# Optimization experiments

Hardware: AMD Instinct MI355X
Metric: run time of the kernel (lower is better)

The kernel has to match this reference:

```python
import jax, jax.numpy as jnp
import numpy as np

DIM = 1024
N_HEADS = 16
HEAD_DIM = DIM // N_HEADS


def setup_inputs() -> dict:
    key = jax.random.key(0)
    ks = jax.random.split(key, 5)
    s = 1.0 / np.sqrt(DIM)
    return {
        "x": jax.random.normal(ks[0], (2, 2048, DIM), dtype=jnp.float32),
        "w_qkv": jax.random.normal(ks[1], (DIM, 3 * DIM), dtype=jnp.float32) * s,
        "b_qkv": jnp.zeros((3 * DIM,), dtype=jnp.float32),
        "w_proj": jax.random.normal(ks[2], (DIM, DIM), dtype=jnp.float32) * s,
        "b_proj": jnp.zeros((DIM,), dtype=jnp.float32),
    }


def reference(x, w_qkv, b_qkv, w_proj, b_proj):
    B, T, C = x.shape
    qkv = x @ w_qkv + b_qkv                      # [B,T,3C]
    qkv = qkv.reshape(B, T, 3, N_HEADS, HEAD_DIM)
    q, k, v = qkv[:, :, 0], qkv[:, :, 1], qkv[:, :, 2]  # [B,T,H,D]
    scale = 1.0 / np.sqrt(HEAD_DIM)
    scores = jnp.einsum("bqhd,bkhd->bhqk", q, k) * scale  # [B,H,T,T]
    attn = jax.nn.softmax(scores, axis=-1)
    out = jnp.einsum("bhqk,bkhd->bqhd", attn, v)          # [B,T,H,D]
    out = out.reshape(B, T, C)
    return out @ w_proj + b_proj
```

## Files before the change

kernel.cpp:

```cpp
#include <hip/hip_runtime.h>

typedef unsigned short u16;
typedef unsigned int   u32;
typedef __bf16 bf16x8 __attribute__((ext_vector_type(8)));
typedef float  f32x4  __attribute__((ext_vector_type(4)));
typedef float  f32x16 __attribute__((ext_vector_type(16)));

#define TSEQ 2048
#define NHEAD 16
#define HDIM 64
#define CDIM 1024
#define N3   3072
#define MROWS 4096

__device__ __forceinline__ u16 f2bf(float f) {
    union { float f; u32 u; } v; v.f = f;
    u32 r = v.u + 0x7FFFu + ((v.u >> 16) & 1u);
    return (u16)(r >> 16);
}

__device__ __forceinline__ u32 pkbf(float a, float b) {
#if __has_builtin(__builtin_amdgcn_cvt_pk_bf16_f32)
    typedef __bf16 bf16x2 __attribute__((ext_vector_type(2)));
    bf16x2 t = __builtin_amdgcn_cvt_pk_bf16_f32(a, b);
    union { bf16x2 v; u32 u; } c; c.v = t; return c.u;
#else
    return (u32)f2bf(a) | ((u32)f2bf(b) << 16);
#endif
}

__device__ __forceinline__ void gld16(const u16* g, u16* l) {
    __builtin_amdgcn_global_load_lds(
        (const __attribute__((address_space(1))) u32*)g,
        (__attribute__((address_space(3))) u32*)l, 16, 0, 0);
}

__global__ __launch_bounds__(256) void pack_bf16_kernel(const float* __restrict__ in,
                                                        u16* __restrict__ out, int n4) {
    int i = blockIdx.x * 256 + threadIdx.x;
    if (i >= n4) return;
    float4 v = reinterpret_cast<const float4*>(in)[i];
    ushort4 o;
    o.x = f2bf(v.x); o.y = f2bf(v.y); o.z = f2bf(v.z); o.w = f2bf(v.w);
    reinterpret_cast<ushort4*>(out)[i] = o;
}

__global__ __launch_bounds__(256) void transpose_pack(const float* __restrict__ in,
                                                      u16* __restrict__ out, int K, int N) {
    __shared__ float tile[32][33];
    int n0 = blockIdx.x * 32, k0 = blockIdx.y * 32;
    int tx = threadIdx.x, ty = threadIdx.y;
#pragma unroll
    for (int i = 0; i < 4; i++)
        tile[ty + i * 8][tx] = in[(size_t)(k0 + ty + i * 8) * N + n0 + tx];
    __syncthreads();
#pragma unroll
    for (int i = 0; i < 4; i++)
        out[(size_t)(n0 + ty + i * 8) * K + k0 + tx] = f2bf(tile[tx][ty + i * 8]);
}

__global__ __launch_bounds__(256) void gemm_qkv(const u16* __restrict__ A, const u16* __restrict__ Bt,
                                                const float* __restrict__ bias, u16* __restrict__ Qb,
                                                u16* __restrict__ Ksw, u16* __restrict__ Vsw) {
    __shared__ __align__(16) u16 Al[128 * 32];
    __shared__ __align__(16) u16 Bl[128 * 32];
    const int tid  = threadIdx.x;
    const int lane = tid & 63;
    const int wave = tid >> 6;
    const int wm = (wave >> 1) * 64;
    const int wn = (wave & 1) * 64;
    const int row0 = blockIdx.x * 128;
    const int col0 = blockIdx.y * 128;
    const int lr = lane & 15;
    const int lq = lane >> 4;
    const float c2 = 0.125f * 1.44269504088896f;

    f32x4 acc[4][4];
#pragma unroll
    for (int i = 0; i < 4; i++)
#pragma unroll
        for (int j = 0; j < 4; j++) acc[i][j] = f32x4{0.f, 0.f, 0.f, 0.f};

    const int sr = tid >> 2, sc_ = (tid & 3) * 8;

    for (int k0 = 0; k0 < CDIM; k0 += 32) {
#pragma unroll
        for (int s = 0; s < 2; s++) {
            int i = tid + s * 256;
            int r = sr + s * 64;
            gld16(&A[(size_t)(row0 + r) * CDIM + k0 + sc_], &Al[i * 8]);
            gld16(&Bt[(size_t)(col0 + r) * CDIM + k0 + sc_], &Bl[i * 8]);
        }
        __syncthreads();
        bf16x8 af[4], bfr[4];
#pragma unroll
        for (int t = 0; t < 4; t++) {
            af[t]  = *reinterpret_cast<const bf16x8*>(&Al[(wm + t * 16 + lr) * 32 + lq * 8]);
            bfr[t] = *reinterpret_cast<const bf16x8*>(&Bl[(wn + t * 16 + lr) * 32 + lq * 8]);
        }
#pragma unroll
        for (int mt = 0; mt < 4; mt++)
#pragma unroll
            for (int nt = 0; nt < 4; nt++)
                acc[mt][nt] = __builtin_amdgcn_mfma_f32_16x16x32_bf16(af[mt], bfr[nt], acc[mt][nt], 0, 0, 0);
        __syncthreads();
    }
#pragma unroll
    for (int mt = 0; mt < 4; mt++) {
#pragma unroll
        for (int nt = 0; nt < 4; nt++) {
            int col = col0 + wn + nt * 16 + lr;
            float bv = bias[col];
            int region = col >> 10;
            int c = col & 1023, h = c >> 6, d = c & 63;
#pragma unroll
            for (int r = 0; r < 4; r++) {
                int m = row0 + wm + mt * 16 + lq * 4 + r;
                float v = acc[mt][nt][r] + bv;
                int b  = m >> 11, t = m & 2047;
                int kb = t >> 6,  tr = t & 63;
                size_t base = (size_t)((b * 16 + h) * 32 + kb) * 4096;
                if (region == 0) {
                    Qb[(size_t)m * 1024 + col] = f2bf(v * c2);
                } else if (region == 1) {
                    Ksw[base + tr * 64 + (((d >> 3) ^ (tr & 7)) << 3) + (d & 7)] = f2bf(v);
                } else {
                    int slot = (tr >> 4) * 16 + ((tr >> 2) & 1) * 8 + (tr & 3) + ((tr >> 3) & 1) * 4;
                    Vsw[base + d * 64 + (((slot >> 3) ^ (d & 7)) << 3) + (slot & 7)] = f2bf(v);
                }
            }
        }
    }
}

__global__ __launch_bounds__(256) void gemm_proj(const u16* __restrict__ A, const u16* __restrict__ Bt,
                                                 const float* __restrict__ bias, float* __restrict__ C) {
    __shared__ __align__(16) u16 Al[64 * 32];
    __shared__ __align__(16) u16 Bl[128 * 32];
    const int tid  = threadIdx.x;
    const int lane = tid & 63;
    const int wave = tid >> 6;
    const int wm = (wave >> 1) * 32;
    const int wn = (wave & 1) * 64;
    const int row0 = blockIdx.x * 64;
    const int col0 = blockIdx.y * 128;
    const int lr = lane & 15;
    const int lq = lane >> 4;

    f32x4 acc[2][4];
#pragma unroll
    for (int i = 0; i < 2; i++)
#pragma unroll
        for (int j = 0; j < 4; j++) acc[i][j] = f32x4{0.f, 0.f, 0.f, 0.f};

    const int sr = tid >> 2, sc_ = (tid & 3) * 8;

    for (int k0 = 0; k0 < CDIM; k0 += 32) {
        gld16(&A[(size_t)(row0 + sr) * CDIM + k0 + sc_], &Al[tid * 8]);
#pragma unroll
        for (int s = 0; s < 2; s++)
            gld16(&Bt[(size_t)(col0 + sr + s * 64) * CDIM + k0 + sc_], &Bl[(tid + s * 256) * 8]);
        __syncthreads();
        bf16x8 af[2], bfr[4];
#pragma unroll
        for (int t = 0; t < 2; t++)
            af[t] = *reinterpret_cast<const bf16x8*>(&Al[(wm + t * 16 + lr) * 32 + lq * 8]);
#pragma unroll
        for (int t = 0; t < 4; t++)
            bfr[t] = *reinterpret_cast<const bf16x8*>(&Bl[(wn + t * 16 + lr) * 32 + lq * 8]);
#pragma unroll
        for (int mt = 0; mt < 2; mt++)
#pragma unroll
            for (int nt = 0; nt < 4; nt++)
                acc[mt][nt] = __builtin_amdgcn_mfma_f32_16x16x32_bf16(af[mt], bfr[nt], acc[mt][nt], 0, 0, 0);
        __syncthreads();
    }
#pragma unroll
    for (int mt = 0; mt < 2; mt++) {
#pragma unroll
        for (int nt = 0; nt < 4; nt++) {
            int col = col0 + wn + nt * 16 + lr;
            float bv = bias[col];
#pragma unroll
            for (int r = 0; r < 4; r++) {
                int row = row0 + wm + mt * 16 + lq * 4 + r;
                C[(size_t)row * CDIM + col] = acc[mt][nt][r] + bv;
            }
        }
    }
}

__global__ __launch_bounds__(256) void attn_kernel(const u16* __restrict__ Qb,
                                                   const u16* __restrict__ Ksw,
                                                   const u16* __restrict__ Vsw,
                                                   u16* __restrict__ AO) {
    __shared__ __align__(16) u16 Kl[2][64 * 64];
    __shared__ __align__(16) u16 Vl[2][64 * 64];
    const int qb = blockIdx.x, h = blockIdx.y, b = blockIdx.z;
    const int tid = threadIdx.x, lane = tid & 63, wave = tid >> 6;
    const int l31 = lane & 31, l5 = lane >> 5;
    const int q0 = qb * 128 + wave * 32;

    bf16x8 qf[4];
    {
        const u16* qp = Qb + (size_t)(b * TSEQ + q0 + l31) * CDIM + h * 64 + l5 * 8;
#pragma unroll
        for (int kc = 0; kc < 4; kc++) qf[kc] = *reinterpret_cast<const bf16x8*>(qp + kc * 16);
    }
    f32x16 o[2];
#pragma unroll
    for (int dt = 0; dt < 2; dt++)
#pragma unroll
        for (int i = 0; i < 16; i++) o[dt][i] = 0.f;
    float l = 0.f;

    const u16* ktiles = Ksw + (size_t)((b * 16 + h) * 32) * 4096;
    const u16* vtiles = Vsw + (size_t)((b * 16 + h) * 32) * 4096;
    const int soff = tid * 8;

#pragma unroll
    for (int j = 0; j < 2; j++) {
        gld16(ktiles + j * 2048 + soff, &Kl[0][j * 2048 + soff]);
        gld16(vtiles + j * 2048 + soff, &Vl[0][j * 2048 + soff]);
    }
    __syncthreads();

    for (int kb = 0; kb < TSEQ / 64; kb++) {
        const int cur = kb & 1, nxt = cur ^ 1;
        const int nkb = (kb + 1 < TSEQ / 64) ? kb + 1 : kb;
#pragma unroll
        for (int j = 0; j < 2; j++) {
            gld16(ktiles + (size_t)nkb * 4096 + j * 2048 + soff, &Kl[nxt][j * 2048 + soff]);
            gld16(vtiles + (size_t)nkb * 4096 + j * 2048 + soff, &Vl[nxt][j * 2048 + soff]);
        }
        f32x16 st[2];
#pragma unroll
        for (int nt = 0; nt < 2; nt++)
#pragma unroll
            for (int i = 0; i < 16; i++) st[nt][i] = 0.f;
#pragma unroll
        for (int kc = 0; kc < 4; kc++) {
#pragma unroll
            for (int nt = 0; nt < 2; nt++) {
                bf16x8 kf = *reinterpret_cast<const bf16x8*>(
                    &Kl[cur][(nt * 32 + l31) * 64 + (((kc * 2 + l5) ^ (l31 & 7)) << 3)]);
                st[nt] = __builtin_amdgcn_mfma_f32_32x32x16_bf16(kf, qf[kc], st[nt], 0, 0, 0);
            }
        }
        bf16x8 pa[4];
#pragma unroll
        for (int nt = 0; nt < 2; nt++) {
            float pe[16];
#pragma unroll
            for (int r = 0; r < 16; r++) {
                pe[r] = __builtin_amdgcn_exp2f(st[nt][r]);
                l += pe[r];
            }
            union { bf16x8 v; u32 w[4]; } u0, u1;
#pragma unroll
            for (int j = 0; j < 4; j++) {
                u0.w[j] = pkbf(pe[2 * j],     pe[2 * j + 1]);
                u1.w[j] = pkbf(pe[8 + 2 * j], pe[8 + 2 * j + 1]);
            }
            pa[nt * 2]     = u0.v;
            pa[nt * 2 + 1] = u1.v;
        }
#pragma unroll
        for (int c = 0; c < 4; c++) {
#pragma unroll
            for (int dt = 0; dt < 2; dt++) {
                bf16x8 vf = *reinterpret_cast<const bf16x8*>(
                    &Vl[cur][(dt * 32 + l31) * 64 + (((c * 2 + l5) ^ (l31 & 7)) << 3)]);
                o[dt] = __builtin_amdgcn_mfma_f32_32x32x16_bf16(pa[c], vf, o[dt], 0, 0, 0);
            }
        }
        __syncthreads();
    }
    l += __shfl_xor(l, 32);
    float linv = 1.0f / l;
#pragma unroll
    for (int reg = 0; reg < 16; reg++) {
        int qrow = (reg & 3) + 8 * (reg >> 2) + 4 * l5;
        float li = __shfl(linv, qrow);
#pragma unroll
        for (int dt = 0; dt < 2; dt++) {
            AO[(size_t)(b * TSEQ + q0 + qrow) * CDIM + h * 64 + dt * 32 + l31] =
                f2bf(o[dt][reg] * li);
        }
    }
}

extern "C" void kernel_launch(void* const* d_in, const int* in_sizes, int n_in,
                              void* d_out, int out_size, void* d_ws, size_t ws_size,
                              hipStream_t stream) {
    const float* x      = (const float*)d_in[0];
    const float* w_qkv  = (const float*)d_in[1];
    const float* b_qkv  = (const float*)d_in[2];
    const float* w_proj = (const float*)d_in[3];
    const float* b_proj = (const float*)d_in[4];
    float* out = (float*)d_out;

    u16* ws     = (u16*)d_ws;
    u16* Xb     = ws;
    u16* Wqkvt  = Xb + 4194304;
    u16* Wprojt = Wqkvt + 3145728;
    u16* Qb     = Wprojt + 1048576;
    u16* Ksw    = Qb + 4194304;
    u16* Vsw    = Ksw + 4194304;
    u16* AO     = Vsw + 4194304;

    pack_bf16_kernel<<<4096, 256, 0, stream>>>(x, Xb, 4194304 / 4);
    transpose_pack<<<dim3(96, 32), dim3(32, 8), 0, stream>>>(w_qkv, Wqkvt, 1024, 3072);
    transpose_pack<<<dim3(32, 32), dim3(32, 8), 0, stream>>>(w_proj, Wprojt, 1024, 1024);
    gemm_qkv<<<dim3(32, 24), 256, 0, stream>>>(Xb, Wqkvt, b_qkv, Qb, Ksw, Vsw);
    attn_kernel<<<dim3(16, 16, 2), 256, 0, stream>>>(Qb, Ksw, Vsw, AO);
    gemm_proj<<<dim3(64, 8), 256, 0, stream>>>(AO, Wprojt, b_proj, out);
}
```

Before: 199.7 us.

## Store Q/K/V in MFMA-fragment order and load attention operands directly to registers

The QKV GEMM epilogue now writes Q, K and V in a layout that matches the per-lane MFMA fragment order. This lets the attention kernel drop its LDS double-buffering and block-wide barriers and load K/V fragments straight from global memory into registers, with K prefetched one tile ahead. Each wave now reads the full K/V stream itself instead of sharing it through LDS, which raises global/L2 traffic and register pressure. The change also merges the two weight-transpose launches into one, reorders the attention grid so heads are the fastest-varying index, and adds a v_perm fallback for bf16 packing.

```diff
diff --git a/kernel.cpp b/kernel.cpp
--- a/kernel.cpp
+++ b/kernel.cpp
@@ -25,7 +25,10 @@
     bf16x2 t = __builtin_amdgcn_cvt_pk_bf16_f32(a, b);
     union { bf16x2 v; u32 u; } c; c.v = t; return c.u;
 #else
-    return (u32)f2bf(a) | ((u32)f2bf(b) << 16);
+    union { float f; u32 u; } ua, ub; ua.f = a; ub.f = b;
+    u32 sel = 0x07060302, d;
+    asm("v_perm_b32 %0, %1, %2, %3" : "=v"(d) : "v"(ub.u), "v"(ua.u), "v"(sel));
+    return d;
 #endif
 }
 
@@ -45,10 +48,15 @@
     reinterpret_cast<ushort4*>(out)[i] = o;
 }
 
-__global__ __launch_bounds__(256) void transpose_pack(const float* __restrict__ in,
-                                                      u16* __restrict__ out, int K, int N) {
+__global__ __launch_bounds__(256) void transpose_pack2(const float* __restrict__ wqkv,
+                                                       const float* __restrict__ wproj,
+                                                       u16* __restrict__ oqkv, u16* __restrict__ oproj) {
     __shared__ float tile[32][33];
-    int n0 = blockIdx.x * 32, k0 = blockIdx.y * 32;
+    const int bx = blockIdx.x;
+    const float* in; u16* out; int N, n0;
+    if (bx < 96) { in = wqkv;  out = oqkv;  N = 3072; n0 = bx * 32; }
+    else         { in = wproj; out = oproj; N = 1024; n0 = (bx - 96) * 32; }
+    int k0 = blockIdx.y * 32;
     int tx = threadIdx.x, ty = threadIdx.y;
 #pragma unroll
     for (int i = 0; i < 4; i++)
@@ -56,12 +64,12 @@
     __syncthreads();
 #pragma unroll
     for (int i = 0; i < 4; i++)
-        out[(size_t)(n0 + ty + i * 8) * K + k0 + tx] = f2bf(tile[tx][ty + i * 8]);
+        out[(size_t)(n0 + ty + i * 8) * 1024 + k0 + tx] = f2bf(tile[tx][ty + i * 8]);
 }
 
 __global__ __launch_bounds__(256) void gemm_qkv(const u16* __restrict__ A, const u16* __restrict__ Bt,
-                                                const float* __restrict__ bias, u16* __restrict__ Qb,
-                                                u16* __restrict__ Ksw, u16* __restrict__ Vsw) {
+                                                const float* __restrict__ bias, u16* __restrict__ Qf,
+                                                u16* __restrict__ Kf, u16* __restrict__ Vf) {
     __shared__ __align__(16) u16 Al[128 * 32];
     __shared__ __align__(16) u16 Bl[128 * 32];
     const int tid  = threadIdx.x;
@@ -112,21 +120,31 @@
             int col = col0 + wn + nt * 16 + lr;
             float bv = bias[col];
             int region = col >> 10;
-            int c = col & 1023, h = c >> 6, d = c & 63;
+            int c1 = col & 1023;
+            int h2 = c1 >> 6, d = c1 & 63;
 #pragma unroll
             for (int r = 0; r < 4; r++) {
                 int m = row0 + wm + mt * 16 + lq * 4 + r;
                 float v = acc[mt][nt][r] + bv;
-                int b  = m >> 11, t = m & 2047;
-                int kb = t >> 6,  tr = t & 63;
-                size_t base = (size_t)((b * 16 + h) * 32 + kb) * 4096;
+                int bq = m >> 11, q = m & 2047;
                 if (region == 0) {
-                    Qb[(size_t)m * 1024 + col] = f2bf(v * c2);
-                } else if (region == 1) {
-                    Ksw[base + tr * 64 + (((d >> 3) ^ (tr & 7)) << 3) + (d & 7)] = f2bf(v);
+                    int kc = d >> 4, l5b = (d >> 3) & 1, j = d & 7;
+                    size_t off = ((size_t)((bq * 16 + h2) * 64 + (q >> 5)) * 4 + kc) * 512
+                               + (l5b * 32 + (q & 31)) * 8 + j;
+                    Qf[off] = f2bf(v * c2);
                 } else {
-                    int slot = (tr >> 4) * 16 + ((tr >> 2) & 1) * 8 + (tr & 3) + ((tr >> 3) & 1) * 4;
-                    Vsw[base + d * 64 + (((slot >> 3) ^ (d & 7)) << 3) + (slot & 7)] = f2bf(v);
+                    int kb = q >> 6, tr = q & 63;
+                    size_t tb = (size_t)((bq * 16 + h2) * 32 + kb) * 4096;
+                    if (region == 1) {
+                        int kc = d >> 4, l5b = (d >> 3) & 1, j = d & 7;
+                        int nt2 = tr >> 5, p31 = tr & 31;
+                        Kf[tb + ((kc * 2 + nt2) * 64 + l5b * 32 + p31) * 8 + j] = f2bf(v);
+                    } else {
+                        int cV = tr >> 4, dt = d >> 5, p31 = d & 31;
+                        int l5b = (tr >> 2) & 1;
+                        int j = ((tr >> 3) & 1) * 4 + (tr & 3);
+                        Vf[tb + ((cV * 2 + dt) * 64 + l5b * 32 + p31) * 8 + j] = f2bf(v);
+                    }
                 }
             }
         }
@@ -190,63 +208,55 @@
     }
 }
 
-__global__ __launch_bounds__(256) void attn_kernel(const u16* __restrict__ Qb,
-                                                   const u16* __restrict__ Ksw,
-                                                   const u16* __restrict__ Vsw,
+__global__ __launch_bounds__(256) void attn_kernel(const u16* __restrict__ Qf,
+                                                   const u16* __restrict__ Kf,
+                                                   const u16* __restrict__ Vf,
                                                    u16* __restrict__ AO) {
-    __shared__ __align__(16) u16 Kl[2][64 * 64];
-    __shared__ __align__(16) u16 Vl[2][64 * 64];
-    const int qb = blockIdx.x, h = blockIdx.y, b = blockIdx.z;
+    const int id = blockIdx.x;
+    const int bh = id & 31;
+    const int qb = id >> 5;
+    const int b = bh >> 4, h = bh & 15;
     const int tid = threadIdx.x, lane = tid & 63, wave = tid >> 6;
     const int l31 = lane & 31, l5 = lane >> 5;
-    const int q0 = qb * 128 + wave * 32;
+    const int qt = qb * 4 + wave;
+    const int q0 = qt * 32;
 
     bf16x8 qf[4];
     {
-        const u16* qp = Qb + (size_t)(b * TSEQ + q0 + l31) * CDIM + h * 64 + l5 * 8;
-#pragma unroll
-        for (int kc = 0; kc < 4; kc++) qf[kc] = *reinterpret_cast<const bf16x8*>(qp + kc * 16);
+        const u16* qp = Qf + ((size_t)(bh * 64 + qt) * 4) * 512 + lane * 8;
+#pragma unroll
+        for (int kc = 0; kc < 4; kc++) qf[kc] = *reinterpret_cast<const bf16x8*>(qp + kc * 512);
     }
     f32x16 o[2];
-#pragma unroll
-    for (int dt = 0; dt < 2; dt++)
-#pragma unroll
-        for (int i = 0; i < 16; i++) o[dt][i] = 0.f;
+    f32x16 zc;
+#pragma unroll
+    for (int i = 0; i < 16; i++) { o[0][i] = 0.f; o[1][i] = 0.f; zc[i] = 0.f; }
     float l = 0.f;
 
-    const u16* ktiles = Ksw + (size_t)((b * 16 + h) * 32) * 4096;
-    const u16* vtiles = Vsw + (size_t)((b * 16 + h) * 32) * 4096;
-    const int soff = tid * 8;
-
-#pragma unroll
-    for (int j = 0; j < 2; j++) {
-        gld16(ktiles + j * 2048 + soff, &Kl[0][j * 2048 + soff]);
-        gld16(vtiles + j * 2048 + soff, &Vl[0][j * 2048 + soff]);
-    }
-    __syncthreads();
-
-    for (int kb = 0; kb < TSEQ / 64; kb++) {
-        const int cur = kb & 1, nxt = cur ^ 1;
-        const int nkb = (kb + 1 < TSEQ / 64) ? kb + 1 : kb;
-#pragma unroll
-        for (int j = 0; j < 2; j++) {
-            gld16(ktiles + (size_t)nkb * 4096 + j * 2048 + soff, &Kl[nxt][j * 2048 + soff]);
-            gld16(vtiles + (size_t)nkb * 4096 + j * 2048 + soff, &Vl[nxt][j * 2048 + soff]);
-        }
+    const u16* kcur = Kf + (size_t)bh * 32 * 4096 + lane * 8;
+    const u16* vcur = Vf + (size_t)bh * 32 * 4096 + lane * 8;
+
+    bf16x8 ka[8];
+#pragma unroll
+    for (int i = 0; i < 8; i++) ka[i] = *reinterpret_cast<const bf16x8*>(kcur + i * 512);
+
+    for (int kb = 0; kb < 32; kb++) {
         f32x16 st[2];
-#pragma unroll
-        for (int nt = 0; nt < 2; nt++)
-#pragma unroll
-            for (int i = 0; i < 16; i++) st[nt][i] = 0.f;
-#pragma unroll
-        for (int kc = 0; kc < 4; kc++) {
-#pragma unroll
-            for (int nt = 0; nt < 2; nt++) {
-                bf16x8 kf = *reinterpret_cast<const bf16x8*>(
-                    &Kl[cur][(nt * 32 + l31) * 64 + (((kc * 2 + l5) ^ (l31 & 7)) << 3)]);
-                st[nt] = __builtin_amdgcn_mfma_f32_32x32x16_bf16(kf, qf[kc], st[nt], 0, 0, 0);
-            }
-        }
+        st[0] = __builtin_amdgcn_mfma_f32_32x32x16_bf16(ka[0], qf[0], zc, 0, 0, 0);
+        st[1] = __builtin_amdgcn_mfma_f32_32x32x16_bf16(ka[1], qf[0], zc, 0, 0, 0);
+#pragma unroll
+        for (int kc = 1; kc < 4; kc++) {
+            st[0] = __builtin_amdgcn_mfma_f32_32x32x16_bf16(ka[kc * 2],     qf[kc], st[0], 0, 0, 0);
+            st[1] = __builtin_amdgcn_mfma_f32_32x32x16_bf16(ka[kc * 2 + 1], qf[kc], st[1], 0, 0, 0);
+        }
+        bf16x8 vfr[8];
+#pragma unroll
+        for (int i = 0; i < 8; i++) vfr[i] = *reinterpret_cast<const bf16x8*>(vcur + i * 512);
+        const u16* knext = kcur + (kb < 31 ? 4096 : 0);
+#pragma unroll
+        for (int i = 0; i < 8; i++) ka[i] = *reinterpret_cast<const bf16x8*>(knext + i * 512);
+        kcur = knext;
+        vcur += 4096;
         bf16x8 pa[4];
 #pragma unroll
         for (int nt = 0; nt < 2; nt++) {
@@ -267,14 +277,9 @@
         }
 #pragma unroll
         for (int c = 0; c < 4; c++) {
-#pragma unroll
-            for (int dt = 0; dt < 2; dt++) {
-                bf16x8 vf = *reinterpret_cast<const bf16x8*>(
-                    &Vl[cur][(dt * 32 + l31) * 64 + (((c * 2 + l5) ^ (l31 & 7)) << 3)]);
-                o[dt] = __builtin_amdgcn_mfma_f32_32x32x16_bf16(pa[c], vf, o[dt], 0, 0, 0);
-            }
-        }
-        __syncthreads();
+            o[0] = __builtin_amdgcn_mfma_f32_32x32x16_bf16(pa[c], vfr[c * 2],     o[0], 0, 0, 0);
+            o[1] = __builtin_amdgcn_mfma_f32_32x32x16_bf16(pa[c], vfr[c * 2 + 1], o[1], 0, 0, 0);
+        }
     }
     l += __shfl_xor(l, 32);
     float linv = 1.0f / l;
@@ -304,15 +309,14 @@
     u16* Xb     = ws;
     u16* Wqkvt  = Xb + 4194304;
     u16* Wprojt = Wqkvt + 3145728;
-    u16* Qb     = Wprojt + 1048576;
-    u16* Ksw    = Qb + 4194304;
-    u16* Vsw    = Ksw + 4194304;
-    u16* AO     = Vsw + 4194304;
+    u16* Qf     = Wprojt + 1048576;
+    u16* Kf     = Qf + 4194304;
+    u16* Vf     = Kf + 4194304;
+    u16* AO     = Vf + 4194304;
 
     pack_bf16_kernel<<<4096, 256, 0, stream>>>(x, Xb, 4194304 / 4);
-    transpose_pack<<<dim3(96, 32), dim3(32, 8), 0, stream>>>(w_qkv, Wqkvt, 1024, 3072);
-    transpose_pack<<<dim3(32, 32), dim3(32, 8), 0, stream>>>(w_proj, Wprojt, 1024, 1024);
-    gemm_qkv<<<dim3(32, 24), 256, 0, stream>>>(Xb, Wqkvt, b_qkv, Qb, Ksw, Vsw);
-    attn_kernel<<<dim3(16, 16, 2), 256, 0, stream>>>(Qb, Ksw, Vsw, AO);
+    transpose_pack2<<<dim3(128, 32), dim3(32, 8), 0, stream>>>(w_qkv, w_proj, Wqkvt, Wprojt);
+    gemm_qkv<<<dim3(32, 24), 256, 0, stream>>>(Xb, Wqkvt, b_qkv, Qf, Kf, Vf);
+    attn_kernel<<<512, 256, 0, stream>>>(Qf, Kf, Vf, AO);
     gemm_proj<<<dim3(64, 8), 256, 0, stream>>>(AO, Wprojt, b_proj, out);
 }
```

Measured after the change: 185.3 us. 1.08x faster.
